# Optimization experiments

Measured on AMD Instinct MI355X. Metric: run time of the kernel, lower is better.

## Reference

```python
import jax, jax.numpy as jnp
import numpy as np

B, H, S, D1, D2 = 1, 8, 4096, 64, 64


def setup_inputs() -> dict:
    key = jax.random.key(0)
    ks = jax.random.split(key, 6)
    q = jax.random.normal(ks[0], (B, H, S, D1), dtype=jnp.float32)
    k = jax.random.normal(ks[1], (B, H, S, D1), dtype=jnp.float32)
    v = jax.random.normal(ks[2], (B, H, S, D2), dtype=jnp.float32)
    # Decay coefficients per head/position (positive, like RetNet gamma^i masks)
    coef_q = jax.random.uniform(ks[3], (H, S), dtype=jnp.float32)
    coef_k = jax.random.uniform(ks[4], (H, S), dtype=jnp.float32)
    # Normalizer must be bounded away from 0
    mask_normer = jax.random.uniform(ks[5], (H, S), dtype=jnp.float32) + 0.5
    return {"q": q, "k": k, "v": v, "coef_q": coef_q, "coef_k": coef_k,
            "mask_normer": mask_normer}


def _rmsenorm(x):
    return x * jax.lax.rsqrt(jnp.mean(x * x, axis=-1, keepdims=True) + 1e-6)


def reference(q, k, v, coef_q, coef_k, mask_normer):
    # q,k: [B,H,S,D1]; v: [B,H,S,D2]; coef_*/mask_normer: [H,S]
    q_bar = q * (coef_q / mask_normer)[None, :, :, None]      # [B,H,S,D1]
    k_bar = k * coef_k[None, :, :, None]                       # [B,H,S,D1]
    # running normalization P_i = |q_i . sum_{j<=i} k_j|, clamped at 1
    T = jnp.cumsum(k_bar, axis=-2)                             # [B,H,S,D1]
    P = jnp.einsum('bhid,bhid->bhi', T, q_bar)                 # [B,H,S]
    P = jnp.maximum(jnp.abs(jax.lax.stop_gradient(P)), 1.0)[..., None]
    q_bar = q_bar / P
    # outer-product state and prefix sum over sequence
    D = jnp.einsum('bhia,bhic->bhiac', k_bar, v)               # [B,H,S,D1,D2]
    D = jnp.cumsum(D, axis=-3)                                 # cumsum over S
    O = jnp.einsum('bhia,bhiac->bhic', q_bar, D)               # [B,H,S,D2]
    return _rmsenorm(O)
```

## Files before the change

kernel.cpp:

```cpp
#include <hip/hip_runtime.h>

#define H 8
#define S 4096
#define D 64
#define C 64
#define NC (S / C)
#define PITCH 72
#define FP 68

typedef short bf16x8 __attribute__((ext_vector_type(8)));
typedef float f32x4 __attribute__((ext_vector_type(4)));
typedef unsigned uint4v __attribute__((ext_vector_type(4)));

struct alignas(16) F4 { float v[4]; };

__device__ inline short rne_bf16(float x) {
  unsigned u = __builtin_bit_cast(unsigned, x);
  unsigned r = u + 0x7fffu + ((u >> 16) & 1u);
  return (short)(r >> 16);
}
__device__ inline float bf16_to_f(short h) {
  unsigned u = ((unsigned)(unsigned short)h) << 16;
  return __builtin_bit_cast(float, u);
}

__global__ __launch_bounds__(256) void k_chunk_sums(
    const float* __restrict__ k, const float* __restrict__ v,
    const float* __restrict__ coef_k, float* __restrict__ wsKV) {
  const int ch = blockIdx.x, h = blockIdx.y, t = threadIdx.x;
  __shared__ float kb[C * FP];
  __shared__ float vb[C * FP];
  __shared__ alignas(16) short kT[D * PITCH];
  __shared__ alignas(16) short vT[D * PITCH];

  const float* kp = k + (size_t)(h * S + ch * C) * D;
  const float* vp = v + (size_t)(h * S + ch * C) * D;
  const float* ck = coef_k + h * S + ch * C;

#pragma unroll
  for (int r = 0; r < 4; ++r) {
    int o = 1024 * r + 4 * t;
    int i = o >> 6, d = o & 63;
    F4 kv = *reinterpret_cast<const F4*>(kp + o);
    F4 vv = *reinterpret_cast<const F4*>(vp + o);
    float c = ck[i];
#pragma unroll
    for (int u = 0; u < 4; ++u) kv.v[u] *= c;
    *reinterpret_cast<F4*>(&kb[i * FP + d]) = kv;
    *reinterpret_cast<F4*>(&vb[i * FP + d]) = vv;
  }
  __syncthreads();

  {
    const int col = t & 63, i0 = 16 * (t >> 6);
    bf16x8 wk[2], wv[2];
#pragma unroll
    for (int g = 0; g < 2; ++g)
#pragma unroll
      for (int u = 0; u < 8; ++u) {
        wk[g][u] = rne_bf16(kb[(i0 + 8 * g + u) * FP + col]);
        wv[g][u] = rne_bf16(vb[(i0 + 8 * g + u) * FP + col]);
      }
    *reinterpret_cast<bf16x8*>(&kT[col * PITCH + i0]) = wk[0];
    *reinterpret_cast<bf16x8*>(&kT[col * PITCH + i0 + 8]) = wk[1];
    *reinterpret_cast<bf16x8*>(&vT[col * PITCH + i0]) = wv[0];
    *reinterpret_cast<bf16x8*>(&vT[col * PITCH + i0 + 8]) = wv[1];
  }
  __syncthreads();

  const int lane = t & 63, w = t >> 6;
  const int arow = lane & 15, kg = lane >> 4;
  const int abase = (16 * w + arow) * PITCH + 8 * kg;
  bf16x8 a0 = *reinterpret_cast<const bf16x8*>(&vT[abase]);
  bf16x8 a1 = *reinterpret_cast<const bf16x8*>(&vT[abase + 32]);
  float* dst = wsKV + (size_t)(h * NC + ch) * (D * D);
#pragma unroll
  for (int n = 0; n < 4; ++n) {
    const int bb = (16 * n + arow) * PITCH + 8 * kg;
    bf16x8 b0 = *reinterpret_cast<const bf16x8*>(&kT[bb]);
    bf16x8 b1 = *reinterpret_cast<const bf16x8*>(&kT[bb + 32]);
    f32x4 z = {0.f, 0.f, 0.f, 0.f};
    z = __builtin_amdgcn_mfma_f32_16x16x32_bf16(a0, b0, z, 0, 0, 0);
    z = __builtin_amdgcn_mfma_f32_16x16x32_bf16(a1, b1, z, 0, 0, 0);
#pragma unroll
    for (int r = 0; r < 4; ++r)
      dst[(16 * w + 4 * kg + r) * D + 16 * n + arow] = z[r];
  }
}

__global__ __launch_bounds__(128) void k_scan(float* __restrict__ wsKV) {
  const int seg = blockIdx.x, h = blockIdx.y, t = threadIdx.x;
  const int e0 = seg * 128 + t;
  unsigned* wp = reinterpret_cast<unsigned*>(wsKV);
  float run = 0.f;
  for (int base = 0; base < NC; base += 16) {
    float x[16];
#pragma unroll
    for (int u = 0; u < 16; ++u)
      x[u] = wsKV[(size_t)(h * NC + base + u) * (D * D) + e0];
#pragma unroll
    for (int u = 0; u < 16; ++u) {
      short hi = rne_bf16(run);
      short lo = rne_bf16(run - bf16_to_f(hi));
      wp[(size_t)(h * NC + base + u) * (D * D) + e0] =
          (((unsigned)(unsigned short)lo) << 16) | (unsigned)(unsigned short)hi;
      run += x[u];
    }
  }
}

__global__ __launch_bounds__(256) void k_chunk_out(
    const float* __restrict__ q, const float* __restrict__ k,
    const float* __restrict__ v,
    const float* __restrict__ coef_q, const float* __restrict__ coef_k,
    const float* __restrict__ mask_normer,
    const float* __restrict__ wsKV, float* __restrict__ out) {
  const int ch = blockIdx.x, h = blockIdx.y, t = threadIdx.x;
  __shared__ alignas(16) short qb[C * PITCH];
  __shared__ alignas(16) short kbf[C * PITCH];
  __shared__ alignas(16) short s0h[D * PITCH];
  __shared__ alignas(16) short s0l[D * PITCH];
  __shared__ alignas(16) short vT[D * PITCH];
  __shared__ alignas(16) short Ab[C * PITCH];
  __shared__ float vb[C * FP];

  const size_t base = (size_t)(h * S + ch * C) * D;
  const float* qp = q + base;
  const float* kp = k + base;
  const float* vp = v + base;
  const float* cq = coef_q + h * S + ch * C;
  const float* ck = coef_k + h * S + ch * C;
  const float* mn = mask_normer + h * S + ch * C;
  const unsigned* s0p =
      reinterpret_cast<const unsigned*>(wsKV) + (size_t)(h * NC + ch) * (D * D);

  {
    const int i = t >> 2, c0 = (t & 3) * 16;
    const float sq = cq[i] / mn[i];
    const float sk = ck[i];
    bf16x8 wq[2], wk[2], wh[2], wl[2];
#pragma unroll
    for (int g = 0; g < 2; ++g) {
#pragma unroll
      for (int u0 = 0; u0 < 8; u0 += 4) {
        F4 qv = *reinterpret_cast<const F4*>(qp + i * D + c0 + 8 * g + u0);
        F4 kv = *reinterpret_cast<const F4*>(kp + i * D + c0 + 8 * g + u0);
#pragma unroll
        for (int u = 0; u < 4; ++u) {
          wq[g][u0 + u] = rne_bf16(qv.v[u] * sq);
          wk[g][u0 + u] = rne_bf16(kv.v[u] * sk);
        }
      }
      uint4v p = *reinterpret_cast<const uint4v*>(s0p + i * D + c0 + 8 * g);
      uint4v p2 = *reinterpret_cast<const uint4v*>(s0p + i * D + c0 + 8 * g + 4);
#pragma unroll
      for (int u = 0; u < 4; ++u) {
        wh[g][u] = (short)(p[u] & 0xffffu);
        wl[g][u] = (short)(p[u] >> 16);
        wh[g][u + 4] = (short)(p2[u] & 0xffffu);
        wl[g][u + 4] = (short)(p2[u] >> 16);
      }
      F4 v0 = *reinterpret_cast<const F4*>(vp + i * D + c0 + 8 * g);
      F4 v1 = *reinterpret_cast<const F4*>(vp + i * D + c0 + 8 * g + 4);
      *reinterpret_cast<F4*>(&vb[i * FP + c0 + 8 * g]) = v0;
      *reinterpret_cast<F4*>(&vb[i * FP + c0 + 8 * g + 4]) = v1;
    }
#pragma unroll
    for (int g = 0; g < 2; ++g) {
      *reinterpret_cast<bf16x8*>(&qb[i * PITCH + c0 + 8 * g]) = wq[g];
      *reinterpret_cast<bf16x8*>(&kbf[i * PITCH + c0 + 8 * g]) = wk[g];
      *reinterpret_cast<bf16x8*>(&s0h[i * PITCH + c0 + 8 * g]) = wh[g];
      *reinterpret_cast<bf16x8*>(&s0l[i * PITCH + c0 + 8 * g]) = wl[g];
    }
  }
  __syncthreads();

  {
    const int col = t & 63, j0 = 16 * (t >> 6);
    bf16x8 wv[2];
#pragma unroll
    for (int g = 0; g < 2; ++g)
#pragma unroll
      for (int u = 0; u < 8; ++u)
        wv[g][u] = rne_bf16(vb[(j0 + 8 * g + u) * FP + col]);
    *reinterpret_cast<bf16x8*>(&vT[col * PITCH + j0]) = wv[0];
    *reinterpret_cast<bf16x8*>(&vT[col * PITCH + j0 + 8]) = wv[1];
  }

  const int lane = t & 63, w = t >> 6;
  const int arow = lane & 15, kg = lane >> 4;
  const int rbase = (16 * w + arow) * PITCH + 8 * kg;

  bf16x8 qa0 = *reinterpret_cast<const bf16x8*>(&qb[rbase]);
  bf16x8 qa1 = *reinterpret_cast<const bf16x8*>(&qb[rbase + 32]);

  {
    f32x4 accA[4];
#pragma unroll
    for (int n = 0; n < 4; ++n) {
      const int bb = (16 * n + arow) * PITCH + 8 * kg;
      bf16x8 b0 = *reinterpret_cast<const bf16x8*>(&kbf[bb]);
      bf16x8 b1 = *reinterpret_cast<const bf16x8*>(&kbf[bb + 32]);
      f32x4 z = {0.f, 0.f, 0.f, 0.f};
      z = __builtin_amdgcn_mfma_f32_16x16x32_bf16(qa0, b0, z, 0, 0, 0);
      z = __builtin_amdgcn_mfma_f32_16x16x32_bf16(qa1, b1, z, 0, 0, 0);
      accA[n] = z;
    }
#pragma unroll
    for (int n = 0; n < 4; ++n)
#pragma unroll
      for (int r = 0; r < 4; ++r) {
        int i = 4 * kg + r;
        int j = 16 * n + arow;
        float x = (j <= 16 * w + i) ? accA[n][r] : 0.f;
        Ab[(16 * w + i) * PITCH + j] = rne_bf16(x);
      }
  }
  __syncthreads();

  bf16x8 aa0 = *reinterpret_cast<const bf16x8*>(&Ab[rbase]);
  bf16x8 aa1 = *reinterpret_cast<const bf16x8*>(&Ab[rbase + 32]);
  f32x4 accO[4];
#pragma unroll
  for (int n = 0; n < 4; ++n) {
    const int bb = (16 * n + arow) * PITCH + 8 * kg;
    bf16x8 h0 = *reinterpret_cast<const bf16x8*>(&s0h[bb]);
    bf16x8 h1 = *reinterpret_cast<const bf16x8*>(&s0h[bb + 32]);
    bf16x8 l0 = *reinterpret_cast<const bf16x8*>(&s0l[bb]);
    bf16x8 l1 = *reinterpret_cast<const bf16x8*>(&s0l[bb + 32]);
    bf16x8 v0 = *reinterpret_cast<const bf16x8*>(&vT[bb]);
    bf16x8 v1 = *reinterpret_cast<const bf16x8*>(&vT[bb + 32]);
    f32x4 z = {0.f, 0.f, 0.f, 0.f};
    z = __builtin_amdgcn_mfma_f32_16x16x32_bf16(qa0, h0, z, 0, 0, 0);
    z = __builtin_amdgcn_mfma_f32_16x16x32_bf16(qa1, h1, z, 0, 0, 0);
    z = __builtin_amdgcn_mfma_f32_16x16x32_bf16(qa0, l0, z, 0, 0, 0);
    z = __builtin_amdgcn_mfma_f32_16x16x32_bf16(qa1, l1, z, 0, 0, 0);
    z = __builtin_amdgcn_mfma_f32_16x16x32_bf16(aa0, v0, z, 0, 0, 0);
    z = __builtin_amdgcn_mfma_f32_16x16x32_bf16(aa1, v1, z, 0, 0, 0);
    accO[n] = z;
  }

  float* op = out + base;
#pragma unroll
  for (int r = 0; r < 4; ++r) {
    const int i = 16 * w + 4 * kg + r;
    float ss = 0.f;
#pragma unroll
    for (int n = 0; n < 4; ++n) ss += accO[n][r] * accO[n][r];
#pragma unroll
    for (int off = 1; off < 16; off <<= 1) ss += __shfl_xor(ss, off);
    const float sc = rsqrtf(ss * (1.0f / D) + 1e-6f);
#pragma unroll
    for (int n = 0; n < 4; ++n)
      op[(size_t)i * D + 16 * n + arow] = accO[n][r] * sc;
  }
}

extern "C" void kernel_launch(void* const* d_in, const int* in_sizes, int n_in,
                              void* d_out, int out_size, void* d_ws, size_t ws_size,
                              hipStream_t stream) {
  (void)in_sizes; (void)n_in; (void)out_size; (void)ws_size;
  const float* q  = (const float*)d_in[0];
  const float* k  = (const float*)d_in[1];
  const float* v  = (const float*)d_in[2];
  const float* cq = (const float*)d_in[3];
  const float* ck = (const float*)d_in[4];
  const float* mn = (const float*)d_in[5];
  float* out = (float*)d_out;

  float* wsKV = (float*)d_ws;

  k_chunk_sums<<<dim3(NC, H), dim3(256), 0, stream>>>(k, v, ck, wsKV);
  k_scan<<<dim3(32, H), dim3(128), 0, stream>>>(wsKV);
  k_chunk_out<<<dim3(NC, H), dim3(256), 0, stream>>>(q, k, v, cq, ck, mn, wsKV, out);
}
```

Before: 25.62 us.

## Store chunk states in bf16 and load transposed tiles directly from global

The per-chunk KV outer-product sums and their prefix scan are now kept as single bf16 values instead of fp32 sums with hi/lo bf16 pairs. This halves workspace traffic in all three kernels and drops two MFMAs per output tile. Global-to-LDS loading of K and V now writes the transposed bf16 tiles directly, removing an fp32 staging buffer, and one __syncthreads that only guarded same-wave data is dropped. The cost is lower accuracy: the scan accumulates bf16-rounded chunk sums and the carried state loses its low-order correction term.

```diff
diff --git a/kernel.cpp b/kernel.cpp
--- a/kernel.cpp
+++ b/kernel.cpp
@@ -6,7 +6,6 @@
 #define C 64
 #define NC (S / C)
 #define PITCH 72
-#define FP 68
 
 typedef short bf16x8 __attribute__((ext_vector_type(8)));
 typedef float f32x4 __attribute__((ext_vector_type(4)));
@@ -14,22 +13,19 @@
 
 struct alignas(16) F4 { float v[4]; };
 
-__device__ inline short rne_bf16(float x) {
+__device__ inline unsigned short rne_bf16(float x) {
   unsigned u = __builtin_bit_cast(unsigned, x);
   unsigned r = u + 0x7fffu + ((u >> 16) & 1u);
-  return (short)(r >> 16);
-}
-__device__ inline float bf16_to_f(short h) {
-  unsigned u = ((unsigned)(unsigned short)h) << 16;
-  return __builtin_bit_cast(float, u);
+  return (unsigned short)(r >> 16);
+}
+__device__ inline float bf16_to_f(unsigned hw) {
+  return __builtin_bit_cast(float, hw << 16);
 }
 
 __global__ __launch_bounds__(256) void k_chunk_sums(
     const float* __restrict__ k, const float* __restrict__ v,
-    const float* __restrict__ coef_k, float* __restrict__ wsKV) {
+    const float* __restrict__ coef_k, unsigned short* __restrict__ wsKV) {
   const int ch = blockIdx.x, h = blockIdx.y, t = threadIdx.x;
-  __shared__ float kb[C * FP];
-  __shared__ float vb[C * FP];
   __shared__ alignas(16) short kT[D * PITCH];
   __shared__ alignas(16) short vT[D * PITCH];
 
@@ -37,43 +33,34 @@
   const float* vp = v + (size_t)(h * S + ch * C) * D;
   const float* ck = coef_k + h * S + ch * C;
 
-#pragma unroll
-  for (int r = 0; r < 4; ++r) {
-    int o = 1024 * r + 4 * t;
-    int i = o >> 6, d = o & 63;
-    F4 kv = *reinterpret_cast<const F4*>(kp + o);
-    F4 vv = *reinterpret_cast<const F4*>(vp + o);
-    float c = ck[i];
-#pragma unroll
-    for (int u = 0; u < 4; ++u) kv.v[u] *= c;
-    *reinterpret_cast<F4*>(&kb[i * FP + d]) = kv;
-    *reinterpret_cast<F4*>(&vb[i * FP + d]) = vv;
+  const int w = t >> 6, col = t & 63;
+  {
+    const int i0 = (w & 1) * 32;
+    const bool isK = (w < 2);
+    const float* src = isK ? kp : vp;
+    short* dstT = isK ? kT : vT;
+    unsigned pr[16];
+#pragma unroll
+    for (int u2 = 0; u2 < 16; ++u2) {
+      float x0 = src[(i0 + 2 * u2) * D + col];
+      float x1 = src[(i0 + 2 * u2 + 1) * D + col];
+      if (isK) { x0 *= ck[i0 + 2 * u2]; x1 *= ck[i0 + 2 * u2 + 1]; }
+      pr[u2] = (unsigned)rne_bf16(x0) | ((unsigned)rne_bf16(x1) << 16);
+    }
+#pragma unroll
+    for (int g = 0; g < 4; ++g) {
+      uint4v wv = {pr[4 * g], pr[4 * g + 1], pr[4 * g + 2], pr[4 * g + 3]};
+      *reinterpret_cast<uint4v*>(&dstT[col * PITCH + i0 + 8 * g]) = wv;
+    }
   }
   __syncthreads();
 
-  {
-    const int col = t & 63, i0 = 16 * (t >> 6);
-    bf16x8 wk[2], wv[2];
-#pragma unroll
-    for (int g = 0; g < 2; ++g)
-#pragma unroll
-      for (int u = 0; u < 8; ++u) {
-        wk[g][u] = rne_bf16(kb[(i0 + 8 * g + u) * FP + col]);
-        wv[g][u] = rne_bf16(vb[(i0 + 8 * g + u) * FP + col]);
-      }
-    *reinterpret_cast<bf16x8*>(&kT[col * PITCH + i0]) = wk[0];
-    *reinterpret_cast<bf16x8*>(&kT[col * PITCH + i0 + 8]) = wk[1];
-    *reinterpret_cast<bf16x8*>(&vT[col * PITCH + i0]) = wv[0];
-    *reinterpret_cast<bf16x8*>(&vT[col * PITCH + i0 + 8]) = wv[1];
-  }
-  __syncthreads();
-
-  const int lane = t & 63, w = t >> 6;
+  const int lane = t & 63;
   const int arow = lane & 15, kg = lane >> 4;
   const int abase = (16 * w + arow) * PITCH + 8 * kg;
   bf16x8 a0 = *reinterpret_cast<const bf16x8*>(&vT[abase]);
   bf16x8 a1 = *reinterpret_cast<const bf16x8*>(&vT[abase + 32]);
-  float* dst = wsKV + (size_t)(h * NC + ch) * (D * D);
+  unsigned short* dst = wsKV + (size_t)(h * NC + ch) * (D * D);
 #pragma unroll
   for (int n = 0; n < 4; ++n) {
     const int bb = (16 * n + arow) * PITCH + 8 * kg;
@@ -84,27 +71,25 @@
     z = __builtin_amdgcn_mfma_f32_16x16x32_bf16(a1, b1, z, 0, 0, 0);
 #pragma unroll
     for (int r = 0; r < 4; ++r)
-      dst[(16 * w + 4 * kg + r) * D + 16 * n + arow] = z[r];
-  }
-}
-
-__global__ __launch_bounds__(128) void k_scan(float* __restrict__ wsKV) {
+      dst[(16 * w + 4 * kg + r) * D + 16 * n + arow] = rne_bf16(z[r]);
+  }
+}
+
+__global__ __launch_bounds__(64) void k_scan(unsigned* __restrict__ wsKV) {
   const int seg = blockIdx.x, h = blockIdx.y, t = threadIdx.x;
-  const int e0 = seg * 128 + t;
-  unsigned* wp = reinterpret_cast<unsigned*>(wsKV);
-  float run = 0.f;
-  for (int base = 0; base < NC; base += 16) {
-    float x[16];
-#pragma unroll
-    for (int u = 0; u < 16; ++u)
-      x[u] = wsKV[(size_t)(h * NC + base + u) * (D * D) + e0];
-#pragma unroll
-    for (int u = 0; u < 16; ++u) {
-      short hi = rne_bf16(run);
-      short lo = rne_bf16(run - bf16_to_f(hi));
-      wp[(size_t)(h * NC + base + u) * (D * D) + e0] =
-          (((unsigned)(unsigned short)lo) << 16) | (unsigned)(unsigned short)hi;
-      run += x[u];
+  const int e0 = seg * 64 + t;
+  float run0 = 0.f, run1 = 0.f;
+  for (int base = 0; base < NC; base += 32) {
+    unsigned x[32];
+#pragma unroll
+    for (int u = 0; u < 32; ++u)
+      x[u] = wsKV[(size_t)(h * NC + base + u) * 2048 + e0];
+#pragma unroll
+    for (int u = 0; u < 32; ++u) {
+      wsKV[(size_t)(h * NC + base + u) * 2048 + e0] =
+          (unsigned)rne_bf16(run0) | ((unsigned)rne_bf16(run1) << 16);
+      run0 += bf16_to_f(x[u] & 0xffffu);
+      run1 += bf16_to_f(x[u] >> 16);
     }
   }
 }
@@ -114,15 +99,13 @@
     const float* __restrict__ v,
     const float* __restrict__ coef_q, const float* __restrict__ coef_k,
     const float* __restrict__ mask_normer,
-    const float* __restrict__ wsKV, float* __restrict__ out) {
+    const unsigned short* __restrict__ wsKV, float* __restrict__ out) {
   const int ch = blockIdx.x, h = blockIdx.y, t = threadIdx.x;
   __shared__ alignas(16) short qb[C * PITCH];
   __shared__ alignas(16) short kbf[C * PITCH];
-  __shared__ alignas(16) short s0h[D * PITCH];
-  __shared__ alignas(16) short s0l[D * PITCH];
+  __shared__ alignas(16) short s0b[D * PITCH];
   __shared__ alignas(16) short vT[D * PITCH];
   __shared__ alignas(16) short Ab[C * PITCH];
-  __shared__ float vb[C * FP];
 
   const size_t base = (size_t)(h * S + ch * C) * D;
   const float* qp = q + base;
@@ -131,61 +114,47 @@
   const float* cq = coef_q + h * S + ch * C;
   const float* ck = coef_k + h * S + ch * C;
   const float* mn = mask_normer + h * S + ch * C;
-  const unsigned* s0p =
-      reinterpret_cast<const unsigned*>(wsKV) + (size_t)(h * NC + ch) * (D * D);
+  const unsigned short* s0p = wsKV + (size_t)(h * NC + ch) * (D * D);
 
   {
     const int i = t >> 2, c0 = (t & 3) * 16;
     const float sq = cq[i] / mn[i];
     const float sk = ck[i];
-    bf16x8 wq[2], wk[2], wh[2], wl[2];
 #pragma unroll
     for (int g = 0; g < 2; ++g) {
+      bf16x8 wq, wk;
 #pragma unroll
       for (int u0 = 0; u0 < 8; u0 += 4) {
         F4 qv = *reinterpret_cast<const F4*>(qp + i * D + c0 + 8 * g + u0);
         F4 kv = *reinterpret_cast<const F4*>(kp + i * D + c0 + 8 * g + u0);
 #pragma unroll
         for (int u = 0; u < 4; ++u) {
-          wq[g][u0 + u] = rne_bf16(qv.v[u] * sq);
-          wk[g][u0 + u] = rne_bf16(kv.v[u] * sk);
+          wq[u0 + u] = (short)rne_bf16(qv.v[u] * sq);
+          wk[u0 + u] = (short)rne_bf16(kv.v[u] * sk);
         }
       }
-      uint4v p = *reinterpret_cast<const uint4v*>(s0p + i * D + c0 + 8 * g);
-      uint4v p2 = *reinterpret_cast<const uint4v*>(s0p + i * D + c0 + 8 * g + 4);
-#pragma unroll
-      for (int u = 0; u < 4; ++u) {
-        wh[g][u] = (short)(p[u] & 0xffffu);
-        wl[g][u] = (short)(p[u] >> 16);
-        wh[g][u + 4] = (short)(p2[u] & 0xffffu);
-        wl[g][u + 4] = (short)(p2[u] >> 16);
-      }
-      F4 v0 = *reinterpret_cast<const F4*>(vp + i * D + c0 + 8 * g);
-      F4 v1 = *reinterpret_cast<const F4*>(vp + i * D + c0 + 8 * g + 4);
-      *reinterpret_cast<F4*>(&vb[i * FP + c0 + 8 * g]) = v0;
-      *reinterpret_cast<F4*>(&vb[i * FP + c0 + 8 * g + 4]) = v1;
+      *reinterpret_cast<bf16x8*>(&qb[i * PITCH + c0 + 8 * g]) = wq;
+      *reinterpret_cast<bf16x8*>(&kbf[i * PITCH + c0 + 8 * g]) = wk;
+      bf16x8 ws = *reinterpret_cast<const bf16x8*>(s0p + i * D + c0 + 8 * g);
+      *reinterpret_cast<bf16x8*>(&s0b[i * PITCH + c0 + 8 * g]) = ws;
+    }
+  }
+  {
+    const int c = t & 63, i0 = 16 * (t >> 6);
+    unsigned pr[8];
+#pragma unroll
+    for (int u2 = 0; u2 < 8; ++u2) {
+      float x0 = vp[(size_t)(i0 + 2 * u2) * D + c];
+      float x1 = vp[(size_t)(i0 + 2 * u2 + 1) * D + c];
+      pr[u2] = (unsigned)rne_bf16(x0) | ((unsigned)rne_bf16(x1) << 16);
     }
 #pragma unroll
     for (int g = 0; g < 2; ++g) {
-      *reinterpret_cast<bf16x8*>(&qb[i * PITCH + c0 + 8 * g]) = wq[g];
-      *reinterpret_cast<bf16x8*>(&kbf[i * PITCH + c0 + 8 * g]) = wk[g];
-      *reinterpret_cast<bf16x8*>(&s0h[i * PITCH + c0 + 8 * g]) = wh[g];
-      *reinterpret_cast<bf16x8*>(&s0l[i * PITCH + c0 + 8 * g]) = wl[g];
+      uint4v wv = {pr[4 * g], pr[4 * g + 1], pr[4 * g + 2], pr[4 * g + 3]};
+      *reinterpret_cast<uint4v*>(&vT[c * PITCH + i0 + 8 * g]) = wv;
     }
   }
   __syncthreads();
-
-  {
-    const int col = t & 63, j0 = 16 * (t >> 6);
-    bf16x8 wv[2];
-#pragma unroll
-    for (int g = 0; g < 2; ++g)
-#pragma unroll
-      for (int u = 0; u < 8; ++u)
-        wv[g][u] = rne_bf16(vb[(j0 + 8 * g + u) * FP + col]);
-    *reinterpret_cast<bf16x8*>(&vT[col * PITCH + j0]) = wv[0];
-    *reinterpret_cast<bf16x8*>(&vT[col * PITCH + j0 + 8]) = wv[1];
-  }
 
   const int lane = t & 63, w = t >> 6;
   const int arow = lane & 15, kg = lane >> 4;
@@ -213,10 +182,9 @@
         int i = 4 * kg + r;
         int j = 16 * n + arow;
         float x = (j <= 16 * w + i) ? accA[n][r] : 0.f;
-        Ab[(16 * w + i) * PITCH + j] = rne_bf16(x);
+        Ab[(16 * w + i) * PITCH + j] = (short)rne_bf16(x);
       }
   }
-  __syncthreads();
 
   bf16x8 aa0 = *reinterpret_cast<const bf16x8*>(&Ab[rbase]);
   bf16x8 aa1 = *reinterpret_cast<const bf16x8*>(&Ab[rbase + 32]);
@@ -224,17 +192,13 @@
 #pragma unroll
   for (int n = 0; n < 4; ++n) {
     const int bb = (16 * n + arow) * PITCH + 8 * kg;
-    bf16x8 h0 = *reinterpret_cast<const bf16x8*>(&s0h[bb]);
-    bf16x8 h1 = *reinterpret_cast<const bf16x8*>(&s0h[bb + 32]);
-    bf16x8 l0 = *reinterpret_cast<const bf16x8*>(&s0l[bb]);
-    bf16x8 l1 = *reinterpret_cast<const bf16x8*>(&s0l[bb + 32]);
+    bf16x8 h0 = *reinterpret_cast<const bf16x8*>(&s0b[bb]);
+    bf16x8 h1 = *reinterpret_cast<const bf16x8*>(&s0b[bb + 32]);
     bf16x8 v0 = *reinterpret_cast<const bf16x8*>(&vT[bb]);
     bf16x8 v1 = *reinterpret_cast<const bf16x8*>(&vT[bb + 32]);
     f32x4 z = {0.f, 0.f, 0.f, 0.f};
     z = __builtin_amdgcn_mfma_f32_16x16x32_bf16(qa0, h0, z, 0, 0, 0);
     z = __builtin_amdgcn_mfma_f32_16x16x32_bf16(qa1, h1, z, 0, 0, 0);
-    z = __builtin_amdgcn_mfma_f32_16x16x32_bf16(qa0, l0, z, 0, 0, 0);
-    z = __builtin_amdgcn_mfma_f32_16x16x32_bf16(qa1, l1, z, 0, 0, 0);
     z = __builtin_amdgcn_mfma_f32_16x16x32_bf16(aa0, v0, z, 0, 0, 0);
     z = __builtin_amdgcn_mfma_f32_16x16x32_bf16(aa1, v1, z, 0, 0, 0);
     accO[n] = z;
@@ -268,9 +232,9 @@
   const float* mn = (const float*)d_in[5];
   float* out = (float*)d_out;
 
-  float* wsKV = (float*)d_ws;
+  unsigned short* wsKV = (unsigned short*)d_ws;
 
   k_chunk_sums<<<dim3(NC, H), dim3(256), 0, stream>>>(k, v, ck, wsKV);
-  k_scan<<<dim3(32, H), dim3(128), 0, stream>>>(wsKV);
+  k_scan<<<dim3(32, H), dim3(64), 0, stream>>>((unsigned*)d_ws);
   k_chunk_out<<<dim3(NC, H), dim3(256), 0, stream>>>(q, k, v, cq, ck, mn, wsKV, out);
 }
```

New measurement: 25.69 us. Within noise of the previous version (+0.3%).
